# Performance work log

Measured on AMD Instinct MI355X. Metric: run time of the kernel, lower is better.

## Reference

```python
import jax, jax.numpy as jnp
from jax import lax
import numpy as np

B, PEP, MHC, V, H, C, K, NH, FLAT = 1024, 15, 44, 21, 9, 3200, 9, 800, 21 * 59
EPS = 1e-5


def setup_inputs() -> dict:
    key = jax.random.key(0)
    ks = jax.random.split(key, 24)
    n = lambda k, s: jax.random.normal(k, s, dtype=jnp.float32) * 0.05
    inp = {
        'pep': jax.random.normal(ks[0], (B, PEP, V), dtype=jnp.float32),
        'mhc': jax.random.normal(ks[1], (B, MHC, V), dtype=jnp.float32),
        # conv module (bias=True inside CapHLA_EL)
        'W1': n(ks[2], (2 * C, V)), 'b1': n(ks[3], (2 * C,)),
        'Wd': n(ks[4], (C, 1, K)), 'bd': n(ks[5], (C,)),
        'bn1_g': jnp.ones((C,), jnp.float32), 'bn1_b': jnp.zeros((C,), jnp.float32),
        'bn1_m': jnp.zeros((C,), jnp.float32), 'bn1_v': jnp.ones((C,), jnp.float32),
        'W2': n(ks[6], (V, C)), 'b2': n(ks[7], (V,)),
        # shared LayerNorm(vocab_size)
        'ln_g': jnp.ones((V,), jnp.float32), 'ln_b': jnp.zeros((V,), jnp.float32),
        # MHA (bias=False)
        'Wq': n(ks[8], (V, V * H)), 'Wk': n(ks[9], (V, V * H)),
        'Wv': n(ks[10], (V, V * H)), 'Wo': n(ks[11], (V * H, V)),
        # feature selection head
        'Wf1': n(ks[12], (FLAT, NH)), 'bf1': n(ks[13], (NH,)),
        'bn2_g': jnp.ones((NH,), jnp.float32), 'bn2_b': jnp.zeros((NH,), jnp.float32),
        'bn2_m': jnp.zeros((NH,), jnp.float32), 'bn2_v': jnp.ones((NH,), jnp.float32),
        'Wf2': n(ks[14], (NH, 64)), 'bf2': n(ks[15], (64,)),
        'Wf3': n(ks[16], (64, 2)), 'bf3': n(ks[17], (2,)),
    }
    return inp


def _ln(x, g, b):
    m = x.mean(-1, keepdims=True)
    v = x.var(-1, keepdims=True)
    return (x - m) * lax.rsqrt(v + EPS) * g + b


def _forward(pep, mhc, W1, b1, Wd, bd, bn1_g, bn1_b, bn1_m, bn1_v, W2, b2,
             ln_g, ln_b, Wq, Wk, Wv, Wo,
             Wf1, bf1, bn2_g, bn2_b, bn2_m, bn2_v, Wf2, bf2, Wf3, bf3):
    X = jnp.concatenate([pep, mhc], axis=1)  # [B, 59, V]
    residual = X
    # ---- convolution module (channels-first) ----
    x = X.transpose(0, 2, 1)                               # [B, V, L]
    x = jnp.einsum('bcl,oc->bol', x, W1) + b1[None, :, None]   # [B, 2C, L]
    a, g = jnp.split(x, 2, axis=1)
    x = a * jax.nn.sigmoid(g)                              # GLU -> [B, C, L]
    x = lax.conv_general_dilated(x, Wd, window_strides=(1,), padding=[((K - 1) // 2, (K - 1) // 2)],
                                 dimension_numbers=('NCH', 'OIH', 'NCH'),
                                 feature_group_count=C) + bd[None, :, None]
    x = (x - bn1_m[None, :, None]) * lax.rsqrt(bn1_v + EPS)[None, :, None] * bn1_g[None, :, None] + bn1_b[None, :, None]
    x = jax.nn.silu(x)
    x = jnp.einsum('bcl,oc->bol', x, W2) + b2[None, :, None]  # [B, V, L]
    X = _ln(residual + x.transpose(0, 2, 1), ln_g, ln_b)
    residual = X
    # ---- multi-head self-attention (head_dim == V) ----
    Bn, S, D = X.shape
    def heads(W):
        return (X @ W).reshape(Bn, S, H, D).transpose(0, 2, 1, 3)  # [B, H, S, D]
    q, k, v = heads(Wq), heads(Wk), heads(Wv)
    scores = jnp.einsum('bhqd,bhkd->bhqk', q, k) / jnp.sqrt(jnp.float32(D))
    attn = jax.nn.softmax(scores, axis=-1)
    o = jnp.einsum('bhqk,bhkd->bhqd', attn, v)
    o = o.transpose(0, 2, 1, 3).reshape(Bn, S, H * D) @ Wo
    X = _ln(residual + o, ln_g, ln_b)
    # ---- feature selection head ----
    h = X.reshape(Bn, -1) @ Wf1 + bf1
    h = jax.nn.silu(h)
    h = (h - bn2_m) * lax.rsqrt(bn2_v + EPS) * bn2_g + bn2_b
    h = jax.nn.relu(h @ Wf2 + bf2)
    return h @ Wf3 + bf3                                   # [B, 2]


def reference(pep, mhc, W1, b1, Wd, bd, bn1_g, bn1_b, bn1_m, bn1_v, W2, b2,
              ln_g, ln_b, Wq, Wk, Wv, Wo,
              Wf1, bf1, bn2_g, bn2_b, bn2_m, bn2_v, Wf2, bf2, Wf3, bf3):
    return _forward(pep, mhc, W1, b1, Wd, bd, bn1_g, bn1_b, bn1_m, bn1_v, W2, b2,
                    ln_g, ln_b, Wq, Wk, Wv, Wo,
                    Wf1, bf1, bn2_g, bn2_b, bn2_m, bn2_v, Wf2, bf2, Wf3, bf3)
```

## Files before the change

kernel.cpp:

```cpp
#include <hip/hip_runtime.h>
#include <hip/hip_bf16.h>

namespace {

constexpr int B   = 1024;
constexpr int PEP = 15;
constexpr int MHCN = 44;
constexpr int S   = 59;
constexpr int V   = 21;
constexpr int C   = 3200;
constexpr int KW  = 9;
constexpr int H   = 9;
constexpr int NH  = 800;
constexpr int SV  = S * V;
constexpr int HD  = H * V;
constexpr int XF  = 1248;
constexpr float EPSF = 1e-5f;
constexpr int CHALF = 25;
constexpr float NLOG2E = -1.4426950408889634f;

typedef __attribute__((ext_vector_type(8))) short short8;
typedef __attribute__((ext_vector_type(4))) float f32x4;
typedef __attribute__((ext_vector_type(2))) float f32x2;

__device__ __forceinline__ float sigm(float x) {
  return __builtin_amdgcn_rcpf(1.f + __expf(-x));
}
__device__ __forceinline__ unsigned short f2bf(float f) {
  unsigned r;
  asm("v_cvt_pk_bf16_f32 %0, %1, %2" : "=v"(r) : "v"(f), "v"(f));
  return (unsigned short)r;
}
__device__ __forceinline__ unsigned pkbf(float a, float b) {
  unsigned r;
  asm("v_cvt_pk_bf16_f32 %0, %1, %2" : "=v"(r) : "v"(a), "v"(b));
  return r;
}
__device__ __forceinline__ float bflo(unsigned d) {
  union { unsigned u; float f; } v; v.u = d << 16; return v.f;
}
__device__ __forceinline__ float bfhi(unsigned d) {
  union { unsigned u; float f; } v; v.u = d & 0xffff0000u; return v.f;
}

__global__ void k_packW(const float* __restrict__ W1, const float* __restrict__ b1,
                        const float* __restrict__ Wd,
                        const float* __restrict__ bd, const float* __restrict__ g,
                        const float* __restrict__ bb, const float* __restrict__ m,
                        const float* __restrict__ vv, const float* __restrict__ W2,
                        const float* __restrict__ Wq, const float* __restrict__ Wk,
                        const float* __restrict__ Wv, const float* __restrict__ Wo,
                        const float* __restrict__ Wf1,
                        unsigned short* __restrict__ FB1, unsigned short* __restrict__ FB2,
                        unsigned short* __restrict__ FQKV, unsigned short* __restrict__ FWo,
                        unsigned short* __restrict__ FWf1, float* __restrict__ TAP) {
  int id = blockIdx.x * 256 + threadIdx.x;
  if (id < 400 * 64) {
    int tau = id >> 6, l = id & 63;
    int ci = tau >> 3, tt = tau & 7;
    int lr = l & 15, lg = l >> 4;
    bool isg = (tt >= 4);
    int row = (!isg) ? (ci * 64 + tt * 16 + lr) : (C + ci * 64 + (tt - 4) * 16 + lr);
    float sc = isg ? NLOG2E : 1.f;
    for (int j = 0; j < 8; ++j) {
      int k = lg * 8 + j;
      float val = (k < V) ? W1[row * V + k] * sc : (k == V ? b1[row] * sc : 0.f);
      FB1[(size_t)tau * 512 + l * 8 + j] = f2bf(val);
    }
  } else if (id < 38400) {
    int id2 = id - 25600;
    int sg = id2 >> 6, l = id2 & 63;
    int ci = sg >> 2, rem = sg & 3, kt = rem >> 1, nt = rem & 1;
    int lr = l & 15, lg = l >> 4;
    int vc = nt * 16 + lr;
    for (int j = 0; j < 8; ++j) {
      int ch = ci * 64 + kt * 32 + lg * 8 + j;
      float val = (vc < V) ? W2[(size_t)vc * C + ch] : 0.f;
      FB2[(size_t)sg * 512 + l * 8 + j] = f2bf(val);
    }
  } else if (id < 41856) {
    int id2 = id - 38400;
    int tile = id2 >> 6, l = id2 & 63;
    int h = tile / 6, rem = tile - h * 6;
    int mat = rem >> 1, nt = rem & 1;
    int lr = l & 15, kg = l >> 4;
    int dcol = nt * 16 + lr;
    const float* W = (mat == 0) ? Wq : (mat == 1) ? Wk : Wv;
    const float scale = (mat == 0) ? 0.21821789023599236f : 1.f;
    for (int j = 0; j < 8; ++j) {
      int u = kg * 8 + j;
      float val = (u < V && dcol < V) ? W[u * HD + h * V + dcol] * scale : 0.f;
      FQKV[(size_t)tile * 512 + l * 8 + j] = f2bf(val);
    }
  } else if (id < 43008) {
    int id2 = id - 41856;
    int tile = id2 >> 6, l = id2 & 63;
    int h = tile >> 1, nt = tile & 1;
    int lr = l & 15, kg = l >> 4;
    int vcol = nt * 16 + lr;
    for (int j = 0; j < 8; ++j) {
      int d = kg * 8 + j;
      float val = (d < V && vcol < V) ? Wo[(h * V + d) * V + vcol] : 0.f;
      FWo[(size_t)tile * 512 + l * 8 + j] = f2bf(val);
    }
  } else if (id < 46208) {
    int c = id - 43008;
    if (c < C) {
      float sc = g[c] * rsqrtf(vv[c] + EPSF);
      for (int k = 0; k < KW; ++k) TAP[c * 12 + k] = Wd[c * KW + k] * sc;
      TAP[c * 12 + 9]  = (bd[c] - m[c]) * sc + bb[c];
      TAP[c * 12 + 10] = 0.f;
      TAP[c * 12 + 11] = 0.f;
    }
  } else if (id < 46208 + 1950 * 64) {
    int id2 = id - 46208;
    int tile = id2 >> 6, l = id2 & 63;
    int ntg = tile / 39, kk = tile - ntg * 39;
    int lr = l & 15, kg = l >> 4;
    int n = ntg * 16 + lr;
    for (int j = 0; j < 8; ++j) {
      int f = kk * 32 + kg * 8 + j;
      float val = (f < SV) ? Wf1[(size_t)f * NH + n] : 0.f;
      FWf1[(size_t)tile * 512 + l * 8 + j] = f2bf(val);
    }
  }
}

constexpr int GST = 74;

__device__ __forceinline__ void glu_chunk(const unsigned short* fb1p, unsigned* glw0,
                                          short8 ax, int w, int mypos) {
  f32x4 ga[4], gg[4];
#pragma unroll
  for (int tt = 0; tt < 4; ++tt) {
    short8 bf = *reinterpret_cast<const short8*>(fb1p + tt * 512);
    ga[tt] = __builtin_amdgcn_mfma_f32_16x16x32_bf16(ax, bf, (f32x4){0.f, 0.f, 0.f, 0.f}, 0, 0, 0);
  }
#pragma unroll
  for (int tt = 0; tt < 4; ++tt) {
    short8 bf = *reinterpret_cast<const short8*>(fb1p + (4 + tt) * 512);
    gg[tt] = __builtin_amdgcn_mfma_f32_16x16x32_bf16(ax, bf, (f32x4){0.f, 0.f, 0.f, 0.f}, 0, 0, 0);
  }
  if (w < 3) {
#pragma unroll
    for (int tt = 0; tt < 4; ++tt) {
      unsigned* gw = glw0 + tt * (16 * GST / 2);
      float s0 = __builtin_amdgcn_rcpf(1.f + __builtin_amdgcn_exp2f(gg[tt][0]));
      float s1 = __builtin_amdgcn_rcpf(1.f + __builtin_amdgcn_exp2f(gg[tt][1]));
      float s2 = __builtin_amdgcn_rcpf(1.f + __builtin_amdgcn_exp2f(gg[tt][2]));
      float s3 = __builtin_amdgcn_rcpf(1.f + __builtin_amdgcn_exp2f(gg[tt][3]));
      gw[0] = pkbf(ga[tt][0] * s0, ga[tt][1] * s1);
      gw[1] = pkbf(ga[tt][2] * s2, ga[tt][3] * s3);
    }
  } else {
#pragma unroll
    for (int tt = 0; tt < 4; ++tt) {
      unsigned* gw = glw0 + tt * (16 * GST / 2);
      float g0 = (mypos + 0 < S) ? ga[tt][0] * __builtin_amdgcn_rcpf(1.f + __builtin_amdgcn_exp2f(gg[tt][0])) : 0.f;
      float g1 = (mypos + 1 < S) ? ga[tt][1] * __builtin_amdgcn_rcpf(1.f + __builtin_amdgcn_exp2f(gg[tt][1])) : 0.f;
      float g2 = (mypos + 2 < S) ? ga[tt][2] * __builtin_amdgcn_rcpf(1.f + __builtin_amdgcn_exp2f(gg[tt][2])) : 0.f;
      float g3 = (mypos + 3 < S) ? ga[tt][3] * __builtin_amdgcn_rcpf(1.f + __builtin_amdgcn_exp2f(gg[tt][3])) : 0.f;
      gw[0] = pkbf(g0, g1);
      gw[1] = pkbf(g2, g3);
    }
  }
}

__device__ __forceinline__ void conv_chunk(const unsigned* glr, const float* tapp,
                                           const unsigned short* fb2p,
                                           unsigned short* sbw, const unsigned short* sbr,
                                           int w, f32x4 (&acc2)[2]) {
  const float4 t0 = *reinterpret_cast<const float4*>(tapp);
  const float4 t1 = *reinterpret_cast<const float4*>(tapp + 4);
  const float4 t2 = *reinterpret_cast<const float4*>(tapp + 8);
  const float tap[9] = {t0.x, t0.y, t0.z, t0.w, t1.x, t1.y, t1.z, t1.w, t2.x};
  const float sh = t2.y;
  float gv[24];
#pragma unroll
  for (int i2 = 0; i2 < 12; ++i2) {
    const unsigned d = glr[i2];
    gv[2 * i2]     = bflo(d);
    gv[2 * i2 + 1] = bfhi(d);
  }
  f32x2 q[16];
#pragma unroll
  for (int j = 0; j < 16; ++j) q[j] = (f32x2){gv[j], gv[j + 8]};
#pragma unroll
  for (int i2 = 0; i2 < 8; ++i2) {
    f32x2 ac = (f32x2){sh, sh};
#pragma unroll
    for (int k = 0; k < KW; ++k) {
      f32x2 tk = (f32x2){tap[k], tap[k]};
      ac = ac + q[i2 + k] * tk;
    }
    const float a0 = ac.x, a1 = ac.y;
    const float s0 = a0 * __builtin_amdgcn_rcpf(1.f + __builtin_amdgcn_exp2f(a0 * NLOG2E));
    const float s1 = a1 * __builtin_amdgcn_rcpf(1.f + __builtin_amdgcn_exp2f(a1 * NLOG2E));
    sbw[i2 * 72] = f2bf(s0);
    unsigned short hv = f2bf(s1);
    if (w == 3 && i2 >= 3) hv = 0;
    sbw[(i2 + 8) * 72] = hv;
  }
#pragma unroll
  for (int kt = 0; kt < 2; ++kt) {
    short8 a2f = *reinterpret_cast<const short8*>(sbr + kt * 32);
#pragma unroll
    for (int nt = 0; nt < 2; ++nt) {
      short8 b2f = *reinterpret_cast<const short8*>(fb2p + (kt * 2 + nt) * 512);
      acc2[nt] = __builtin_amdgcn_mfma_f32_16x16x32_bf16(a2f, b2f, acc2[nt], 0, 0, 0);
    }
  }
}

__global__ __launch_bounds__(256) void k_conv(
    const float* __restrict__ pep, const float* __restrict__ mhc,
    const unsigned short* __restrict__ FB1, const unsigned short* __restrict__ FB2,
    const float* __restrict__ TAP, float* __restrict__ Yp) {
  __shared__ __align__(16) unsigned char smem[2 * 64 * GST * 2 + 4 * 16 * 72 * 2];
  unsigned short* Xbf = reinterpret_cast<unsigned short*>(smem);
  unsigned short* glA = reinterpret_cast<unsigned short*>(smem);
  unsigned short* glB = glA + 64 * GST;
  unsigned short* Sb  = glB + 64 * GST;
  const int t = threadIdx.x;
  const int b = blockIdx.x >> 1;
  const int half = blockIdx.x & 1;
  const int lane = t & 63;
  const int w = t >> 6;
  const int lr = lane & 15;
  const int lg = lane >> 4;

  {
    const int row = t >> 2, q = t & 3;
    const float* xr = (row < PEP) ? pep + ((size_t)b * PEP + row) * V
                    : (row < S)   ? mhc + ((size_t)b * MHCN + (row - PEP)) * V
                                  : nullptr;
#pragma unroll
    for (int i2 = 0; i2 < 5; ++i2) {
      int c0 = q * 10 + 2 * i2;
      float f0 = (xr && c0 < V) ? xr[c0] : 0.f;
      float f1 = (xr && c0 + 1 < V) ? xr[c0 + 1] : ((xr && c0 + 1 == V) ? 1.f : 0.f);
      *reinterpret_cast<unsigned*>(&Xbf[row * 40 + c0]) = pkbf(f0, f1);
    }
  }
  __syncthreads();

  short8 ax = *reinterpret_cast<const short8*>(&Xbf[(w * 16 + lr) * 40 + lg * 8]);
  __syncthreads();

  {
    const int i = t;
    unsigned short* buf = (i < 128) ? glA : glB;
    const int i2 = i & 127;
    *reinterpret_cast<unsigned*>(&buf[(i2 >> 1) * GST + (i2 & 1) * 2]) = 0u;
  }

  f32x4 acc2[2];
  acc2[0] = (f32x4){0.f, 0.f, 0.f, 0.f};
  acc2[1] = (f32x4){0.f, 0.f, 0.f, 0.f};
  const int mypos = w * 16 + lg * 4;

  unsigned* glwA = reinterpret_cast<unsigned*>(&glA[lr * GST + 4 + mypos]);
  unsigned* glwB = reinterpret_cast<unsigned*>(&glB[lr * GST + 4 + mypos]);
  const unsigned* glrA = reinterpret_cast<const unsigned*>(&glA[lane * GST + w * 16]);
  const unsigned* glrB = reinterpret_cast<const unsigned*>(&glB[lane * GST + w * 16]);
  unsigned short* sbw = Sb + w * (16 * 72) + lane;
  const unsigned short* sbr = Sb + w * (16 * 72) + lr * 72 + lg * 8;
  const unsigned short* fb1p = FB1 + (size_t)half * CHALF * 8 * 512 + lane * 8;
  const unsigned short* fb2p = FB2 + (size_t)half * CHALF * 4 * 512 + lane * 8;
  const float* tapp = TAP + ((size_t)half * CHALF * 64 + lane) * 12;

  glu_chunk(fb1p, glwA, ax, w, mypos);
  __syncthreads();

  for (int p = 0; p < 12; ++p) {
    glu_chunk(fb1p + 4096, glwB, ax, w, mypos);
    conv_chunk(glrA, tapp, fb2p, sbw, sbr, w, acc2);
    __syncthreads();
    glu_chunk(fb1p + 2 * 4096, glwA, ax, w, mypos);
    conv_chunk(glrB, tapp + 768, fb2p + 2048, sbw, sbr, w, acc2);
    __syncthreads();
    fb1p += 2 * 4096;
    fb2p += 2 * 2048;
    tapp += 2 * 768;
  }
  conv_chunk(glrA, tapp, fb2p, sbw, sbr, w, acc2);

  float* yp = Yp + (size_t)blockIdx.x * SV;
#pragma unroll
  for (int nt = 0; nt < 2; ++nt) {
#pragma unroll
    for (int r = 0; r < 4; ++r) {
      const int pos = mypos + r, vc = nt * 16 + lr;
      if (pos < S && vc < V) yp[pos * V + vc] = acc2[nt][r];
    }
  }
}

__global__ __launch_bounds__(64) void k_ln(
    const float* __restrict__ pep, const float* __restrict__ mhc,
    const float* __restrict__ Yp, const float* __restrict__ b2,
    const float* __restrict__ lng, const float* __restrict__ lnb,
    float* __restrict__ X1) {
  const int t = threadIdx.x;
  const int b = blockIdx.x;
  if (t >= S) return;
  const float* xr = (t < PEP) ? pep + ((size_t)b * PEP + t) * V
                              : mhc + ((size_t)b * MHCN + (t - PEP)) * V;
  const float* y0 = Yp + (size_t)(2 * b) * SV + t * V;
  const float* y1 = y0 + SV;
  float z[V];
  float mn = 0.f;
#pragma unroll
  for (int v = 0; v < V; ++v) {
    z[v] = xr[v] + (y0[v] + y1[v]) + b2[v];
    mn += z[v];
  }
  mn *= (1.f / V);
  float var = 0.f;
#pragma unroll
  for (int v = 0; v < V; ++v) {
    float d = z[v] - mn;
    var = fmaf(d, d, var);
  }
  const float inv = rsqrtf(var * (1.f / V) + EPSF);
#pragma unroll
  for (int v = 0; v < V; ++v)
    X1[(size_t)b * SV + t * V + v] = (z[v] - mn) * inv * lng[v] + lnb[v];
}

__global__ __launch_bounds__(256) void k_attn(
    const float* __restrict__ X1, const unsigned short* __restrict__ FQKV,
    const unsigned short* __restrict__ FWo, const float* __restrict__ lng,
    const float* __restrict__ lnb, unsigned short* __restrict__ X2bf) {
  __shared__ float X1f[64 * 21];
  __shared__ __align__(16) unsigned short Qb[64 * 40];
  __shared__ __align__(16) unsigned short Kb[64 * 40];
  __shared__ __align__(16) unsigned short Vt[32 * 72];
  __shared__ __align__(16) unsigned short Pt[64 * 72];
  __shared__ __align__(16) unsigned short Oh[64 * 40];
  const int t = threadIdx.x;
  const int b = blockIdx.x;
  const int lane = t & 63;
  const int w = t >> 6;
  const int lr = lane & 15;
  const int lg = lane >> 4;
  const int mypos = w * 16 + lg * 4;

  for (int i = t; i < 64 * 21; i += 256)
    X1f[i] = (i < SV) ? X1[(size_t)b * SV + i] : 0.f;
  __syncthreads();

  short8 ax;
  {
    const int rowi = w * 16 + lr;
#pragma unroll
    for (int j = 0; j < 8; ++j) {
      int col = lg * 8 + j;
      ax[j] = (short)((col < V) ? f2bf(X1f[rowi * 21 + col]) : (unsigned short)0);
    }
  }
  f32x4 accw[2];
  accw[0] = (f32x4){0.f, 0.f, 0.f, 0.f};
  accw[1] = (f32x4){0.f, 0.f, 0.f, 0.f};

  for (int h = 0; h < H; ++h) {
    const unsigned short* fq = FQKV + (size_t)(h * 6) * 512;
    f32x4 dq[2], dk[2], dv[2];
#pragma unroll
    for (int nt = 0; nt < 2; ++nt) {
      short8 bq = *reinterpret_cast<const short8*>(fq + (0 + nt) * 512 + lane * 8);
      dq[nt] = __builtin_amdgcn_mfma_f32_16x16x32_bf16(ax, bq, (f32x4){0.f, 0.f, 0.f, 0.f}, 0, 0, 0);
      short8 bk = *reinterpret_cast<const short8*>(fq + (2 + nt) * 512 + lane * 8);
      dk[nt] = __builtin_amdgcn_mfma_f32_16x16x32_bf16(ax, bk, (f32x4){0.f, 0.f, 0.f, 0.f}, 0, 0, 0);
      short8 bv = *reinterpret_cast<const short8*>(fq + (4 + nt) * 512 + lane * 8);
      dv[nt] = __builtin_amdgcn_mfma_f32_16x16x32_bf16(ax, bv, (f32x4){0.f, 0.f, 0.f, 0.f}, 0, 0, 0);
    }
#pragma unroll
    for (int nt = 0; nt < 2; ++nt) {
      const int d = nt * 16 + lr;
#pragma unroll
      for (int r = 0; r < 4; ++r) {
        const int pos = mypos + r;
        Qb[pos * 40 + d] = f2bf(dq[nt][r]);
        Kb[pos * 40 + d] = f2bf(dk[nt][r]);
      }
      *reinterpret_cast<unsigned*>(&Vt[d * 72 + mypos])     = pkbf(dv[nt][0], dv[nt][1]);
      *reinterpret_cast<unsigned*>(&Vt[d * 72 + mypos + 2]) = pkbf(dv[nt][2], dv[nt][3]);
    }
    __syncthreads();

    short8 bqf = *reinterpret_cast<const short8*>(&Qb[(w * 16 + lr) * 40 + lg * 8]);
    f32x4 st[4];
#pragma unroll
    for (int mt = 0; mt < 4; ++mt) {
      short8 akf = *reinterpret_cast<const short8*>(&Kb[(mt * 16 + lr) * 40 + lg * 8]);
      st[mt] = __builtin_amdgcn_mfma_f32_16x16x32_bf16(akf, bqf, (f32x4){0.f, 0.f, 0.f, 0.f}, 0, 0, 0);
    }
    float mx = -1e30f;
#pragma unroll
    for (int mt = 0; mt < 4; ++mt)
#pragma unroll
      for (int r = 0; r < 4; ++r) {
        const int j = mt * 16 + lg * 4 + r;
        float sv = (j < S) ? st[mt][r] : -1e30f;
        st[mt][r] = sv;
        mx = fmaxf(mx, sv);
      }
    mx = fmaxf(mx, __shfl_xor(mx, 16));
    mx = fmaxf(mx, __shfl_xor(mx, 32));
    float sum = 0.f;
#pragma unroll
    for (int mt = 0; mt < 4; ++mt)
#pragma unroll
      for (int r = 0; r < 4; ++r) {
        float e = __expf(st[mt][r] - mx);
        st[mt][r] = e;
        sum += e;
      }
    sum += __shfl_xor(sum, 16);
    sum += __shfl_xor(sum, 32);
#pragma unroll
    for (int mt = 0; mt < 4; ++mt) {
#pragma unroll
      for (int s2 = 0; s2 < 2; ++s2) {
        *reinterpret_cast<unsigned*>(&Pt[(w * 16 + lr) * 72 + mt * 16 + lg * 4 + 2 * s2]) =
            pkbf(st[mt][2 * s2], st[mt][2 * s2 + 1]);
      }
    }
    short8 bp0 = *reinterpret_cast<const short8*>(&Pt[(w * 16 + lr) * 72 + lg * 8]);
    short8 bp1 = *reinterpret_cast<const short8*>(&Pt[(w * 16 + lr) * 72 + 32 + lg * 8]);
    f32x4 ot[2];
    ot[0] = (f32x4){0.f, 0.f, 0.f, 0.f};
    ot[1] = (f32x4){0.f, 0.f, 0.f, 0.f};
#pragma unroll
    for (int mt = 0; mt < 2; ++mt) {
      short8 av0 = *reinterpret_cast<const short8*>(&Vt[(mt * 16 + lr) * 72 + lg * 8]);
      ot[mt] = __builtin_amdgcn_mfma_f32_16x16x32_bf16(av0, bp0, ot[mt], 0, 0, 0);
      short8 av1 = *reinterpret_cast<const short8*>(&Vt[(mt * 16 + lr) * 72 + 32 + lg * 8]);
      ot[mt] = __builtin_amdgcn_mfma_f32_16x16x32_bf16(av1, bp1, ot[mt], 0, 0, 0);
    }
    const float inv = __builtin_amdgcn_rcpf(sum);
#pragma unroll
    for (int mt = 0; mt < 2; ++mt) {
#pragma unroll
      for (int s2 = 0; s2 < 2; ++s2) {
        *reinterpret_cast<unsigned*>(&Oh[(w * 16 + lr) * 40 + mt * 16 + lg * 4 + 2 * s2]) =
            pkbf(ot[mt][2 * s2] * inv, ot[mt][2 * s2 + 1] * inv);
      }
    }
    short8 ao = *reinterpret_cast<const short8*>(&Oh[(w * 16 + lr) * 40 + lg * 8]);
#pragma unroll
    for (int nt = 0; nt < 2; ++nt) {
      short8 bw = *reinterpret_cast<const short8*>(FWo + (size_t)(h * 2 + nt) * 512 + lane * 8);
      accw[nt] = __builtin_amdgcn_mfma_f32_16x16x32_bf16(ao, bw, accw[nt], 0, 0, 0);
    }
    __syncthreads();
  }

#pragma unroll
  for (int r = 0; r < 4; ++r) {
    const int pos = mypos + r;
    const bool v1ok = (lr < 5);
    const float x0 = (pos < S) ? X1f[pos * 21 + lr] : 0.f;
    const float x1 = (v1ok && pos < S) ? X1f[pos * 21 + 16 + lr] : 0.f;
    float z0 = accw[0][r] + x0;
    float z1 = v1ok ? (accw[1][r] + x1) : 0.f;
    float s = z0 + z1;
    s += __shfl_xor(s, 1); s += __shfl_xor(s, 2);
    s += __shfl_xor(s, 4); s += __shfl_xor(s, 8);
    const float mn = s * (1.f / V);
    const float d0 = z0 - mn;
    const float d1 = v1ok ? (z1 - mn) : 0.f;
    float vq = d0 * d0 + d1 * d1;
    vq += __shfl_xor(vq, 1); vq += __shfl_xor(vq, 2);
    vq += __shfl_xor(vq, 4); vq += __shfl_xor(vq, 8);
    const float inv = rsqrtf(vq * (1.f / V) + EPSF);
    if (pos < S) {
      X2bf[(size_t)b * XF + pos * 21 + lr] = f2bf(d0 * inv * lng[lr] + lnb[lr]);
      if (v1ok)
        X2bf[(size_t)b * XF + pos * 21 + 16 + lr] = f2bf(d1 * inv * lng[16 + lr] + lnb[16 + lr]);
    }
  }
  if (t < XF - SV) X2bf[(size_t)b * XF + SV + t] = 0;
}

__global__ __launch_bounds__(256) void k_f1(
    const unsigned short* __restrict__ X2bf, const unsigned short* __restrict__ FWf1,
    const float* __restrict__ bf1, const float* __restrict__ g2,
    const float* __restrict__ bb2, const float* __restrict__ m2,
    const float* __restrict__ v2, float* __restrict__ Hb) {
  const int t = threadIdx.x;
  const int lane = t & 63;
  const int w = t >> 6;
  const int lr = lane & 15;
  const int lg = lane >> 4;
  const int Mb = blockIdx.x * 64;
  const int NbT = blockIdx.y * 5;

  const unsigned short* ap = X2bf + (size_t)(Mb + w * 16 + lr) * XF + lg * 8;
  const unsigned short* bp = FWf1 + (size_t)NbT * 39 * 512 + lane * 8;
  f32x4 acc[5];
#pragma unroll
  for (int nt = 0; nt < 5; ++nt) acc[nt] = (f32x4){0.f, 0.f, 0.f, 0.f};

  for (int kk = 0; kk < 39; ++kk) {
    short8 af = *reinterpret_cast<const short8*>(ap + kk * 32);
#pragma unroll
    for (int nt = 0; nt < 5; ++nt) {
      short8 bf = *reinterpret_cast<const short8*>(bp + ((size_t)nt * 39 + kk) * 512);
      acc[nt] = __builtin_amdgcn_mfma_f32_16x16x32_bf16(af, bf, acc[nt], 0, 0, 0);
    }
  }
#pragma unroll
  for (int nt = 0; nt < 5; ++nt) {
    const int n = (NbT + nt) * 16 + lr;
    const float sc = g2[n] * rsqrtf(v2[n] + EPSF);
    const float sh = bb2[n] - m2[n] * sc;
    const float bias = bf1[n];
#pragma unroll
    for (int r = 0; r < 4; ++r) {
      const int row = Mb + w * 16 + lg * 4 + r;
      float hh = acc[nt][r] + bias;
      hh = fmaf(hh * sigm(hh), sc, sh);
      Hb[(size_t)row * NH + n] = hh;
    }
  }
}

__global__ __launch_bounds__(64) void k_f23(
    const float* __restrict__ Hb, const float* __restrict__ Wf2, const float* __restrict__ bf2,
    const float* __restrict__ Wf3, const float* __restrict__ bf3, float* __restrict__ out) {
  __shared__ __align__(16) float hs[NH];
  const int t = threadIdx.x;
  const int b = blockIdx.x;
  for (int i = t; i < NH; i += 64) hs[i] = Hb[(size_t)b * NH + i];
  __syncthreads();
  float acc = bf2[t];
  for (int n = 0; n < NH; n += 4) {
    const float4 hv = *reinterpret_cast<const float4*>(&hs[n]);
    acc = fmaf(hv.x, Wf2[n * 64 + t], acc);
    acc = fmaf(hv.y, Wf2[(n + 1) * 64 + t], acc);
    acc = fmaf(hv.z, Wf2[(n + 2) * 64 + t], acc);
    acc = fmaf(hv.w, Wf2[(n + 3) * 64 + t], acc);
  }
  const float mid = fmaxf(acc, 0.f);
  float p0 = mid * Wf3[t * 2 + 0];
  float p1 = mid * Wf3[t * 2 + 1];
#pragma unroll
  for (int off = 32; off > 0; off >>= 1) {
    p0 += __shfl_down(p0, off);
    p1 += __shfl_down(p1, off);
  }
  if (t == 0) {
    out[b * 2 + 0] = p0 + bf3[0];
    out[b * 2 + 1] = p1 + bf3[1];
  }
}

}

extern "C" void kernel_launch(void* const* d_in, const int* in_sizes, int n_in,
                              void* d_out, int out_size, void* d_ws, size_t ws_size,
                              hipStream_t stream) {
  const float* pep   = (const float*)d_in[0];
  const float* mhc   = (const float*)d_in[1];
  const float* W1    = (const float*)d_in[2];
  const float* b1    = (const float*)d_in[3];
  const float* Wd    = (const float*)d_in[4];
  const float* bd    = (const float*)d_in[5];
  const float* bn1_g = (const float*)d_in[6];
  const float* bn1_b = (const float*)d_in[7];
  const float* bn1_m = (const float*)d_in[8];
  const float* bn1_v = (const float*)d_in[9];
  const float* W2    = (const float*)d_in[10];
  const float* b2    = (const float*)d_in[11];
  const float* ln_g  = (const float*)d_in[12];
  const float* ln_b  = (const float*)d_in[13];
  const float* Wq    = (const float*)d_in[14];
  const float* Wk    = (const float*)d_in[15];
  const float* Wv    = (const float*)d_in[16];
  const float* Wo    = (const float*)d_in[17];
  const float* Wf1   = (const float*)d_in[18];
  const float* bf1   = (const float*)d_in[19];
  const float* bn2_g = (const float*)d_in[20];
  const float* bn2_b = (const float*)d_in[21];
  const float* bn2_m = (const float*)d_in[22];
  const float* bn2_v = (const float*)d_in[23];
  const float* Wf2   = (const float*)d_in[24];
  const float* bf2   = (const float*)d_in[25];
  const float* Wf3   = (const float*)d_in[26];
  const float* bf3   = (const float*)d_in[27];
  float* out = (float*)d_out;

  float* ws = (float*)d_ws;
  float* X1 = ws;
  unsigned short* X2bf = (unsigned short*)(X1 + (size_t)B * SV);
  float* Hb = (float*)(X2bf + (size_t)B * XF);
  float* TAP = Hb + (size_t)B * NH;
  unsigned short* FB1  = (unsigned short*)(TAP + (size_t)C * 12);
  unsigned short* FB2  = FB1 + (size_t)400 * 512;
  unsigned short* FQKV = FB2 + (size_t)200 * 512;
  unsigned short* FWo  = FQKV + (size_t)54 * 512;
  unsigned short* FWf1 = FWo + (size_t)18 * 512;
  float* Yp = (float*)(FWf1 + (size_t)1950 * 512);

  k_packW<<<669, 256, 0, stream>>>(W1, b1, Wd, bd, bn1_g, bn1_b, bn1_m, bn1_v, W2,
                                   Wq, Wk, Wv, Wo, Wf1, FB1, FB2, FQKV, FWo, FWf1, TAP);
  k_conv<<<2 * B, 256, 0, stream>>>(pep, mhc, FB1, FB2, TAP, Yp);
  k_ln<<<B, 64, 0, stream>>>(pep, mhc, Yp, b2, ln_g, ln_b, X1);
  k_attn<<<B, 256, 0, stream>>>(X1, FQKV, FWo, ln_g, ln_b, X2bf);
  dim3 g5(16, 10);
  k_f1<<<g5, 256, 0, stream>>>(X2bf, FWf1, bf1, bn2_g, bn2_b, bn2_m, bn2_v, Hb);
  k_f23<<<B, 64, 0, stream>>>(Hb, Wf2, bf2, Wf3, bf3, out);
}
```

Before: 253.1 us.

## Warp-specialize k_conv into separate GLU producer and conv consumer warps

```diff
diff --git a/kernel.cpp b/kernel.cpp
--- a/kernel.cpp
+++ b/kernel.cpp
@@ -129,7 +129,7 @@
 constexpr int GST = 74;
 
 __device__ __forceinline__ void glu_chunk(const unsigned short* fb1p, unsigned* glw0,
-                                          short8 ax, int w, int mypos) {
+                                          short8 ax, int mt, int mypos) {
   f32x4 ga[4], gg[4];
 #pragma unroll
   for (int tt = 0; tt < 4; ++tt) {
@@ -141,7 +141,7 @@
     short8 bf = *reinterpret_cast<const short8*>(fb1p + (4 + tt) * 512);
     gg[tt] = __builtin_amdgcn_mfma_f32_16x16x32_bf16(ax, bf, (f32x4){0.f, 0.f, 0.f, 0.f}, 0, 0, 0);
   }
-  if (w < 3) {
+  if (mt < 3) {
 #pragma unroll
     for (int tt = 0; tt < 4; ++tt) {
       unsigned* gw = glw0 + tt * (16 * GST / 2);
@@ -169,7 +169,7 @@
 __device__ __forceinline__ void conv_chunk(const unsigned* glr, const float* tapp,
                                            const unsigned short* fb2p,
                                            unsigned short* sbw, const unsigned short* sbr,
-                                           int w, f32x4 (&acc2)[2]) {
+                                           int mt, f32x4 (&acc2)[2]) {
   const float4 t0 = *reinterpret_cast<const float4*>(tapp);
   const float4 t1 = *reinterpret_cast<const float4*>(tapp + 4);
   const float4 t2 = *reinterpret_cast<const float4*>(tapp + 8);
@@ -198,7 +198,7 @@
     const float s1 = a1 * __builtin_amdgcn_rcpf(1.f + __builtin_amdgcn_exp2f(a1 * NLOG2E));
     sbw[i2 * 72] = f2bf(s0);
     unsigned short hv = f2bf(s1);
-    if (w == 3 && i2 >= 3) hv = 0;
+    if (mt == 3 && i2 >= 3) hv = 0;
     sbw[(i2 + 8) * 72] = hv;
   }
 #pragma unroll
@@ -212,7 +212,7 @@
   }
 }
 
-__global__ __launch_bounds__(256) void k_conv(
+__global__ __launch_bounds__(512) void k_conv(
     const float* __restrict__ pep, const float* __restrict__ mhc,
     const unsigned short* __restrict__ FB1, const unsigned short* __restrict__ FB2,
     const float* __restrict__ TAP, float* __restrict__ Yp) {
@@ -228,8 +228,11 @@
   const int w = t >> 6;
   const int lr = lane & 15;
   const int lg = lane >> 4;
-
-  {
+  const bool isGlu = (w < 4);
+  const int mt = isGlu ? w : (w - 4);
+  const int mypos = mt * 16 + lg * 4;
+
+  if (t < 256) {
     const int row = t >> 2, q = t & 3;
     const float* xr = (row < PEP) ? pep + ((size_t)b * PEP + row) * V
                     : (row < S)   ? mhc + ((size_t)b * MHCN + (row - PEP)) * V
@@ -244,54 +247,54 @@
   }
   __syncthreads();
 
-  short8 ax = *reinterpret_cast<const short8*>(&Xbf[(w * 16 + lr) * 40 + lg * 8]);
+  short8 ax = {};
+  if (isGlu) ax = *reinterpret_cast<const short8*>(&Xbf[(mt * 16 + lr) * 40 + lg * 8]);
   __syncthreads();
 
-  {
-    const int i = t;
-    unsigned short* buf = (i < 128) ? glA : glB;
-    const int i2 = i & 127;
+  if (t < 256) {
+    unsigned short* buf = (t < 128) ? glA : glB;
+    const int i2 = t & 127;
     *reinterpret_cast<unsigned*>(&buf[(i2 >> 1) * GST + (i2 & 1) * 2]) = 0u;
   }
 
   f32x4 acc2[2];
   acc2[0] = (f32x4){0.f, 0.f, 0.f, 0.f};
   acc2[1] = (f32x4){0.f, 0.f, 0.f, 0.f};
-  const int mypos = w * 16 + lg * 4;
 
   unsigned* glwA = reinterpret_cast<unsigned*>(&glA[lr * GST + 4 + mypos]);
   unsigned* glwB = reinterpret_cast<unsigned*>(&glB[lr * GST + 4 + mypos]);
-  const unsigned* glrA = reinterpret_cast<const unsigned*>(&glA[lane * GST + w * 16]);
-  const unsigned* glrB = reinterpret_cast<const unsigned*>(&glB[lane * GST + w * 16]);
-  unsigned short* sbw = Sb + w * (16 * 72) + lane;
-  const unsigned short* sbr = Sb + w * (16 * 72) + lr * 72 + lg * 8;
+  const unsigned* glrA = reinterpret_cast<const unsigned*>(&glA[lane * GST + mt * 16]);
+  const unsigned* glrB = reinterpret_cast<const unsigned*>(&glB[lane * GST + mt * 16]);
+  unsigned short* sbw = Sb + mt * (16 * 72) + lane;
+  const unsigned short* sbr = Sb + mt * (16 * 72) + lr * 72 + lg * 8;
   const unsigned short* fb1p = FB1 + (size_t)half * CHALF * 8 * 512 + lane * 8;
   const unsigned short* fb2p = FB2 + (size_t)half * CHALF * 4 * 512 + lane * 8;
   const float* tapp = TAP + ((size_t)half * CHALF * 64 + lane) * 12;
 
-  glu_chunk(fb1p, glwA, ax, w, mypos);
+  if (isGlu) glu_chunk(fb1p, glwA, ax, mt, mypos);
   __syncthreads();
 
   for (int p = 0; p < 12; ++p) {
-    glu_chunk(fb1p + 4096, glwB, ax, w, mypos);
-    conv_chunk(glrA, tapp, fb2p, sbw, sbr, w, acc2);
+    if (isGlu) glu_chunk(fb1p + 4096, glwB, ax, mt, mypos);
+    else       conv_chunk(glrA, tapp, fb2p, sbw, sbr, mt, acc2);
     __syncthreads();
-    glu_chunk(fb1p + 2 * 4096, glwA, ax, w, mypos);
-    conv_chunk(glrB, tapp + 768, fb2p + 2048, sbw, sbr, w, acc2);
+    if (isGlu) glu_chunk(fb1p + 2 * 4096, glwA, ax, mt, mypos);
+    else       conv_chunk(glrB, tapp + 768, fb2p + 2048, sbw, sbr, mt, acc2);
     __syncthreads();
     fb1p += 2 * 4096;
     fb2p += 2 * 2048;
     tapp += 2 * 768;
   }
-  conv_chunk(glrA, tapp, fb2p, sbw, sbr, w, acc2);
-
-  float* yp = Yp + (size_t)blockIdx.x * SV;
-#pragma unroll
-  for (int nt = 0; nt < 2; ++nt) {
-#pragma unroll
-    for (int r = 0; r < 4; ++r) {
-      const int pos = mypos + r, vc = nt * 16 + lr;
-      if (pos < S && vc < V) yp[pos * V + vc] = acc2[nt][r];
+  if (!isGlu) {
+    conv_chunk(glrA, tapp, fb2p, sbw, sbr, mt, acc2);
+    float* yp = Yp + (size_t)blockIdx.x * SV;
+#pragma unroll
+    for (int nt = 0; nt < 2; ++nt) {
+#pragma unroll
+      for (int r = 0; r < 4; ++r) {
+        const int pos = mypos + r, vc = nt * 16 + lr;
+        if (pos < S && vc < V) yp[pos * V + vc] = acc2[nt][r];
+      }
     }
   }
 }
@@ -606,7 +609,7 @@
 
   k_packW<<<669, 256, 0, stream>>>(W1, b1, Wd, bd, bn1_g, bn1_b, bn1_m, bn1_v, W2,
                                    Wq, Wk, Wv, Wo, Wf1, FB1, FB2, FQKV, FWo, FWf1, TAP);
-  k_conv<<<2 * B, 256, 0, stream>>>(pep, mhc, FB1, FB2, TAP, Yp);
+  k_conv<<<2 * B, 512, 0, stream>>>(pep, mhc, FB1, FB2, TAP, Yp);
   k_ln<<<B, 64, 0, stream>>>(pep, mhc, Yp, b2, ln_g, ln_b, X1);
   k_attn<<<B, 256, 0, stream>>>(X1, FQKV, FWo, ln_g, ln_b, X2bf);
   dim3 g5(16, 10);
```

Result: faster. 245.5 us (-3.0%).
